# Optimization experiments

Hardware: AMD Instinct MI355X
Metric: run time of the kernel (lower is better)

The kernel has to match this reference:

```python
import jax, jax.numpy as jnp
import numpy as np

BETA = 0.25  # VQ commitment cost


def setup_inputs() -> dict:
    key = jax.random.key(0)
    ks = jax.random.split(key, 6)
    B, C, H, W = 4096, 10, 32, 32
    Din, D, K = 3 * H * W, 256, 512
    img = jax.random.normal(ks[0], (B, 3, H, W), jnp.float32)
    label = jax.random.randint(ks[1], (B,), 0, C)
    enc_W = jax.random.normal(ks[2], (C, Din, D), jnp.float32) * (1.0 / np.sqrt(Din))
    enc_b = jnp.zeros((C, D), jnp.float32)
    codebook = jax.random.normal(ks[3], (K, D), jnp.float32)
    dec_W = jax.random.normal(ks[4], (D, Din), jnp.float32) * (1.0 / np.sqrt(D))
    dec_b = jnp.zeros((Din,), jnp.float32)
    return {"img": img, "label": label, "enc_W": enc_W, "enc_b": enc_b,
            "codebook": codebook, "dec_W": dec_W, "dec_b": dec_b}


def reference(img, label, enc_W, enc_b, codebook, dec_W, dec_b):
    B = img.shape[0]
    C = enc_W.shape[0]
    x = img.reshape(B, -1)                                   # [B, Din]
    onehot = jax.nn.one_hot(label, C, dtype=x.dtype)         # [B, C]
    # label-routed per-class encoders: encode with every expert, select by label
    z_all = jnp.einsum('bi,cid->bcd', x, enc_W) + enc_b[None]  # [B, C, D]
    z = jnp.einsum('bcd,bc->bd', z_all, onehot)              # [B, D]
    # --- VQ quantizer (shared) ---
    d2 = (jnp.sum(z * z, -1, keepdims=True)
          - 2.0 * (z @ codebook.T)
          + jnp.sum(codebook * codebook, -1)[None])          # [B, K]
    idx = jnp.argmin(d2, axis=-1)                            # [B]
    q = codebook[idx]                                        # [B, D]
    # per-sample VQ loss (mean over latent dim): codebook + beta*commitment
    cb_l = jnp.mean((jax.lax.stop_gradient(z) - q) ** 2, -1)
    cm_l = jnp.mean((z - jax.lax.stop_gradient(q)) ** 2, -1)
    l = cb_l + BETA * cm_l                                   # [B]
    q_st = z + jax.lax.stop_gradient(q - z)                  # straight-through
    # quantization loss = (sum over activated classes of per-subset mean) / n_activated
    counts = jax.ops.segment_sum(jnp.ones((B,), x.dtype), label, num_segments=C)
    sum_l = jax.ops.segment_sum(l, label, num_segments=C)
    present = counts > 0
    per_class = jnp.where(present, sum_l / jnp.maximum(counts, 1.0), 0.0)
    n_act = jnp.maximum(jnp.sum(present.astype(x.dtype)), 1.0)
    quant = jnp.sum(per_class) / n_act
    # shared decoder; scatter-back is identity here since every label has an expert
    dec = q_st @ dec_W + dec_b                               # [B, Din]
    img_out = dec.reshape(img.shape)
    loss = jnp.mean((img_out - img) ** 2) + quant
    return (loss, img_out)
```

## Files before the change

kernel.cpp:

```cpp
#include <hip/hip_runtime.h>
#include <hip/hip_bf16.h>
#include <stddef.h>
#include <stdint.h>

#define NB   4096
#define NC   10
#define DIN  3072
#define DD   256
#define KCB  512
#define KSPLIT 6
#define KC   (DIN / KSPLIT)
#define TM   128
#define TGRID 42
#define NIT  (KC / 32)

#define PW_C  786432
#define PW_NH 393216
#define PW_KS 65536
#define PW_IT 4096

typedef unsigned short u16;
typedef short s16x8 __attribute__((ext_vector_type(8)));
typedef float f32x4 __attribute__((ext_vector_type(4)));

__device__ inline void f2bf2(float f, u16& h, u16& l) {
    unsigned uf = __builtin_bit_cast(unsigned, f);
    unsigned uh = (uf + 0x7FFFu + ((uf >> 16) & 1u)) >> 16;
    h = (u16)uh;
    float fh = __builtin_bit_cast(float, uh << 16);
    float r = f - fh;
    unsigned ur = __builtin_bit_cast(unsigned, r);
    l = (u16)((ur + 0x7FFFu + ((ur >> 16) & 1u)) >> 16);
}

__device__ __forceinline__ void gl16(const u16* g, u16* l) {
    __builtin_amdgcn_global_load_lds(
        (const __attribute__((address_space(1))) unsigned int*)(uintptr_t)g,
        (__attribute__((address_space(3))) unsigned int*)(unsigned int)(uintptr_t)l,
        16, 0, 0);
}

__global__ __launch_bounds__(256) void k_wtp(
    const int* __restrict__ label, const float* __restrict__ cb,
    const float* __restrict__ encW, const float* __restrict__ dW,
    int* __restrict__ meta, int* __restrict__ order, float* __restrict__ cbn,
    u16* __restrict__ WtH, u16* __restrict__ WtL,
    u16* __restrict__ dWtH, u16* __restrict__ dWtL, float* __restrict__ cbt)
{
    const int t = threadIdx.x;
    const int bid = blockIdx.x;
    if (bid == 0) {
        __shared__ int cnt_s[NC], cur_s[NC], off_s[NC];
        if (t < NC) { cnt_s[t] = 0; cur_s[t] = 0; }
        __syncthreads();
        for (int b = t; b < NB; b += 256) atomicAdd(&cnt_s[label[b]], 1);
        __syncthreads();
        if (t == 0) {
            int o = 0;
            for (int c = 0; c < NC; ++c) {
                off_s[c] = o; meta[c] = cnt_s[c]; meta[32 + c] = o; o += cnt_s[c];
            }
            meta[32 + NC] = o;
            int ntl = 0;
            for (int c = 0; c < NC; ++c)
                for (int r0 = 0; r0 < cnt_s[c]; r0 += TM) {
                    meta[64 + 2 * ntl] = c; meta[65 + 2 * ntl] = r0; ++ntl;
                }
            meta[63] = ntl;
        }
        __syncthreads();
        for (int b = t; b < NB; b += 256) {
            int c = label[b];
            int p = atomicAdd(&cur_s[c], 1);
            order[off_s[c] + p] = b;
        }
        return;
    }
    if (bid <= 2) {
        int k = (bid - 1) * 256 + t;
        if (k < KCB) {
            const float* r = cb + (size_t)k * DD;
            float a = 0.f;
#pragma unroll 4
            for (int i = 0; i < 64; ++i) {
                float4 v = *(const float4*)(r + i * 4);
                a = fmaf(v.x, v.x, fmaf(v.y, v.y, fmaf(v.z, v.z, fmaf(v.w, v.w, a))));
            }
            cbn[k] = a;
        }
        return;
    }
    const int wb = bid - 3;
    const float* src; int lsrc, ldst, k0, n0;
    u16 *dH = nullptr, *dL = nullptr; float* fdst = nullptr;
    int encw_c = -1;
    if (wb < 1920) {
        int c = wb / 192, rem = wb % 192;
        int kt = rem >> 2, nt = rem & 3;
        k0 = kt * 64; n0 = nt * 64;
        src = encW + (size_t)c * DIN * DD;  lsrc = DD;
        encw_c = c; ldst = 0;
    } else if (wb < 2112) {
        int rem = wb - 1920;
        int kt = rem / 48, nt = rem % 48;
        k0 = kt * 64; n0 = nt * 64;
        src = dW; lsrc = DIN;
        dH = dWtH; dL = dWtL; ldst = DD;
    } else {
        int rem = wb - 2112;
        int kt = rem >> 2, nt = rem & 3;
        k0 = kt * 64; n0 = nt * 64;
        src = cb; lsrc = DD;
        fdst = cbt; ldst = KCB;
    }
    __shared__ float tile[64][65];
    const int trow = t >> 4, tc4 = t & 15;
#pragma unroll
    for (int j = 0; j < 4; ++j) {
        int kk = trow * 4 + j;
        float4 v = *(const float4*)&src[(size_t)(k0 + kk) * lsrc + n0 + tc4 * 4];
        tile[kk][tc4 * 4 + 0] = v.x; tile[kk][tc4 * 4 + 1] = v.y;
        tile[kk][tc4 * 4 + 2] = v.z; tile[kk][tc4 * 4 + 3] = v.w;
    }
    __syncthreads();
    const int n = n0 + (t >> 2), q = t & 3;
    if (fdst) {
#pragma unroll
        for (int j = 0; j < 4; ++j) {
            float4 o = {tile[q * 16 + 4 * j + 0][n - n0], tile[q * 16 + 4 * j + 1][n - n0],
                        tile[q * 16 + 4 * j + 2][n - n0], tile[q * 16 + 4 * j + 3][n - n0]};
            *(float4*)&fdst[(size_t)n * ldst + k0 + q * 16 + 4 * j] = o;
        }
        return;
    }
    s16x8 vh0, vh1, vl0, vl1;
#pragma unroll
    for (int i = 0; i < 8; ++i) {
        u16 h, l;
        f2bf2(tile[q * 16 + i][n - n0], h, l);
        vh0[i] = (short)h; vl0[i] = (short)l;
    }
#pragma unroll
    for (int i = 0; i < 8; ++i) {
        u16 h, l;
        f2bf2(tile[q * 16 + 8 + i][n - n0], h, l);
        vh1[i] = (short)h; vl1[i] = (short)l;
    }
    if (encw_c >= 0) {
        const int nh = n >> 7, cg = (n & 127) >> 4, fr2 = n & 15;
        const size_t nbase = (size_t)encw_c * PW_C + (size_t)nh * PW_NH
                           + (size_t)cg * 512 + (size_t)fr2 * 8;
        int ko = (k0 >> 3) + 2 * q;
        {
            int ks2 = ko >> 6, r2 = ko & 63, it2 = r2 >> 2, fg2 = r2 & 3;
            size_t o = nbase + (size_t)ks2 * PW_KS + (size_t)it2 * PW_IT + (size_t)fg2 * 128;
            *(s16x8*)&WtH[o] = vh0; *(s16x8*)&WtL[o] = vl0;
        }
        {
            int ko1 = ko + 1;
            int ks2 = ko1 >> 6, r2 = ko1 & 63, it2 = r2 >> 2, fg2 = r2 & 3;
            size_t o = nbase + (size_t)ks2 * PW_KS + (size_t)it2 * PW_IT + (size_t)fg2 * 128;
            *(s16x8*)&WtH[o] = vh1; *(s16x8*)&WtL[o] = vl1;
        }
        return;
    }
    u16* oH = dH + (size_t)n * ldst + k0 + q * 16;
    u16* oL = dL + (size_t)n * ldst + k0 + q * 16;
    *(s16x8*)oH = vh0; *(s16x8*)(oH + 8) = vh1;
    *(s16x8*)oL = vl0; *(s16x8*)(oL + 8) = vl1;
}

#define ENC_STEP(IT, PB, L0, L1, C0, C1)                                        \
    {                                                                           \
        if ((IT) + 1 < NIT) { asm volatile("s_waitcnt vmcnt(6)" ::: "memory"); } \
        else                { asm volatile("s_waitcnt vmcnt(0)" ::: "memory"); } \
        asm volatile("s_waitcnt lgkmcnt(0)" ::: "memory");                      \
        __builtin_amdgcn_s_barrier();                                           \
        __builtin_amdgcn_sched_barrier(0);                                      \
        s16x8 aH[4], aL[4], bH[4], bL[4];                                       \
        _Pragma("unroll")                                                       \
        for (int mt = 0; mt < 4; ++mt) {                                        \
            aH[mt] = *(const s16x8*)&AsH[(wr * 4 + mt) * 512 + arb];            \
            aL[mt] = *(const s16x8*)&AsL[(wr * 4 + mt) * 512 + arb];            \
        }                                                                       \
        _Pragma("unroll")                                                       \
        for (int ct = 0; ct < 4; ++ct) {                                        \
            bH[ct] = *(const s16x8*)&BsH[PB][ct * 512 + brb];                   \
            bL[ct] = *(const s16x8*)&BsL[PB][ct * 512 + brb];                   \
        }                                                                       \
        asm volatile("s_waitcnt lgkmcnt(0)" ::: "memory");                      \
        __builtin_amdgcn_sched_barrier(0);                                      \
        __builtin_amdgcn_s_barrier();                                           \
        __builtin_amdgcn_sched_barrier(0);                                      \
        if ((IT) + 2 < NIT) {                                                   \
            L0 = *(const float4*)(xp + ((IT) + 2) * 32);                        \
            L1 = *(const float4*)(xp + ((IT) + 2) * 32 + 4);                    \
            __builtin_amdgcn_sched_barrier(0);                                  \
            const u16* g_ = gchunk + (size_t)((IT) + 2) * PW_IT;                \
            u16* l_ = lchunk + (PB) * 8192;                                     \
            _Pragma("unroll")                                                   \
            for (int i = 0; i < 4; ++i) gl16(g_ + i * 512, l_ + i * 512);       \
            __builtin_amdgcn_sched_barrier(0);                                  \
        }                                                                       \
        __builtin_amdgcn_s_setprio(1);                                          \
        _Pragma("unroll")                                                       \
        for (int ct = 0; ct < 4; ++ct) {                                        \
            _Pragma("unroll")                                                   \
            for (int mt = 0; mt < 4; ++mt) {                                    \
                acc[mt][ct] = __builtin_amdgcn_mfma_f32_16x16x32_bf16(aH[mt], bH[ct], acc[mt][ct], 0, 0, 0); \
                acc[mt][ct] = __builtin_amdgcn_mfma_f32_16x16x32_bf16(aL[mt], bH[ct], acc[mt][ct], 0, 0, 0); \
                acc[mt][ct] = __builtin_amdgcn_mfma_f32_16x16x32_bf16(aH[mt], bL[ct], acc[mt][ct], 0, 0, 0); \
            }                                                                   \
        }                                                                       \
        __builtin_amdgcn_s_setprio(0);                                          \
        if ((IT) + 1 < NIT) {                                                   \
            if ((IT) + 2 < NIT) { asm volatile("s_waitcnt vmcnt(10)" ::: "memory"); } \
            else                { asm volatile("s_waitcnt vmcnt(4)"  ::: "memory"); } \
            cvt_store(C0, C1);                                                  \
        }                                                                       \
    }

__global__ __launch_bounds__(512, 2) void k_enc(
    const float* __restrict__ x, const u16* __restrict__ WpH, const u16* __restrict__ WpL,
    const int* __restrict__ order, const int* __restrict__ meta, float* __restrict__ zpart)
{
    const int bid = blockIdx.x;
    const int ks  = bid % KSPLIT;
    const int tid = bid / KSPLIT;
    if (tid >= meta[63]) return;
    const int c    = meta[64 + 2 * tid];
    const int row0 = meta[65 + 2 * tid];
    const int cnt  = meta[c];
    const int off  = meta[32 + c];
    const int kbase = ks * KC;

    __shared__ __align__(16) u16 AsH[4096], AsL[4096];
    __shared__ __align__(16) u16 BsH[2][8192], BsL[2][8192];

    const int t = threadIdx.x;
    const int lane = t & 63;
    const int w    = t >> 6;
    const int wr = w >> 2, wc = w & 3;
    const int fr = lane & 15, fg = lane >> 4;

    const int ar = ((t >> 6) << 4) | (t & 15);
    const int aq = (t >> 4) & 3;
    int lr = row0 + ar; if (lr > cnt - 1) lr = cnt - 1;
    const float* xp = x + (size_t)order[off + lr] * DIN + kbase + aq * 8;
    const int aoffs = t * 8;

    const u16* gchunk = ((w >> 2) ? WpL : WpH)
                      + (size_t)c * PW_C + (size_t)(w & 1) * PW_NH
                      + (size_t)ks * PW_KS + ((w >> 1) & 1) * 2048 + lane * 8;
    u16* lchunk = ((w >> 2) ? &BsL[0][0] : &BsH[0][0])
                + (w & 1) * 4096 + ((w >> 1) & 1) * 2048 + lane * 8;

    f32x4 acc[4][4];
#pragma unroll
    for (int i = 0; i < 4; ++i)
#pragma unroll
        for (int j = 0; j < 4; ++j) acc[i][j] = (f32x4){0.f, 0.f, 0.f, 0.f};

    auto cvt_store = [&](float4 a0, float4 a1) {
        float av[8] = {a0.x, a0.y, a0.z, a0.w, a1.x, a1.y, a1.z, a1.w};
        s16x8 vh, vl;
#pragma unroll
        for (int i = 0; i < 8; ++i) {
            u16 h, l; f2bf2(av[i], h, l);
            vh[i] = (short)h; vl[i] = (short)l;
        }
        *(s16x8*)&AsH[aoffs] = vh;
        *(s16x8*)&AsL[aoffs] = vl;
    };

    const int arb = fg * 128 + fr * 8;
    const int brb = (wc >> 1) * 4096 + (wc & 1) * 2048 + arb;

    float4 sa0, sa1, sb0, sb1;

    sa0 = *(const float4*)xp;
    sa1 = *(const float4*)(xp + 4);
    __builtin_amdgcn_sched_barrier(0);
#pragma unroll
    for (int i = 0; i < 4; ++i) gl16(gchunk + i * 512, lchunk + i * 512);
    __builtin_amdgcn_sched_barrier(0);
    asm volatile("s_waitcnt vmcnt(4)" ::: "memory");
    cvt_store(sa0, sa1);
    __builtin_amdgcn_sched_barrier(0);
    sb0 = *(const float4*)(xp + 32);
    sb1 = *(const float4*)(xp + 36);
    __builtin_amdgcn_sched_barrier(0);
#pragma unroll
    for (int i = 0; i < 4; ++i) gl16(gchunk + PW_IT + i * 512, lchunk + 8192 + i * 512);
    __builtin_amdgcn_sched_barrier(0);

    for (int itp = 0; itp < NIT; itp += 2) {
        ENC_STEP(itp,     0, sa0, sa1, sb0, sb1);
        ENC_STEP(itp + 1, 1, sb0, sb1, sa0, sa1);
    }

    float* zp = zpart + (size_t)ks * NB * DD;
#pragma unroll
    for (int mt = 0; mt < 4; ++mt) {
#pragma unroll
        for (int r = 0; r < 4; ++r) {
            int lrow = row0 + wr * 64 + mt * 16 + fg * 4 + r;
            if (lrow < cnt) {
                int gb = order[off + lrow];
                float* dst = zp + (size_t)gb * DD + wc * 64 + fr;
#pragma unroll
                for (int ct = 0; ct < 4; ++ct)
                    dst[ct * 16] = acc[mt][ct][r];
            }
        }
    }
}

__global__ __launch_bounds__(256, 3) void k_dec(
    const float* __restrict__ cb, const u16* __restrict__ dWtH, const u16* __restrict__ dWtL,
    const float* __restrict__ db, float* __restrict__ dcb)
{
    const int col0 = blockIdx.x * 256;
    const int m0   = blockIdx.y * 64;

    __shared__ u16 AsH[64 * 40], AsL[64 * 40], BsH[256 * 40], BsL[256 * 40];

    const int t = threadIdx.x;
    const int lane = t & 63;
    const int wid  = t >> 6;
    const int wr = wid >> 1, wc = wid & 1;

    const int ar = t >> 2, aq = t & 3;
    const float* ap = cb + (size_t)(m0 + ar) * DD + aq * 8;
    const int bc = t >> 1, bh = t & 1;
    const u16* wH0 = dWtH + (size_t)(col0 + bc) * DD + bh * 16;
    const u16* wH1 = wH0 + (size_t)128 * DD;
    const u16* wL0 = dWtL + (size_t)(col0 + bc) * DD + bh * 16;
    const u16* wL1 = wL0 + (size_t)128 * DD;

    f32x4 acc[2][8];
#pragma unroll
    for (int i = 0; i < 2; ++i)
#pragma unroll
        for (int j = 0; j < 8; ++j) acc[i][j] = (f32x4){0.f, 0.f, 0.f, 0.f};

    const int fr = lane & 15, fg = lane >> 4;
    const int aoff = fg * 8;
    const int awr = ar * 40 + aq * 8;
    const int bw0 = bc * 40 + bh * 16;
    const int bw1 = (bc + 128) * 40 + bh * 16;

    float4 pa0 = *(const float4*)(ap);
    float4 pa1 = *(const float4*)(ap + 4);
    s16x8 ph0 = *(const s16x8*)(wH0);
    s16x8 ph1 = *(const s16x8*)(wH0 + 8);
    s16x8 ph2 = *(const s16x8*)(wH1);
    s16x8 ph3 = *(const s16x8*)(wH1 + 8);
    s16x8 pl0 = *(const s16x8*)(wL0);
    s16x8 pl1 = *(const s16x8*)(wL0 + 8);
    s16x8 pl2 = *(const s16x8*)(wL1);
    s16x8 pl3 = *(const s16x8*)(wL1 + 8);

    for (int it = 0; it < DD / 32; ++it) {
        {
            float av[8] = {pa0.x, pa0.y, pa0.z, pa0.w, pa1.x, pa1.y, pa1.z, pa1.w};
            s16x8 vh, vl;
#pragma unroll
            for (int i = 0; i < 8; ++i) {
                u16 h, l; f2bf2(av[i], h, l);
                vh[i] = (short)h; vl[i] = (short)l;
            }
            *(s16x8*)&AsH[awr] = vh;
            *(s16x8*)&AsL[awr] = vl;
            *(s16x8*)&BsH[bw0]     = ph0;
            *(s16x8*)&BsH[bw0 + 8] = ph1;
            *(s16x8*)&BsH[bw1]     = ph2;
            *(s16x8*)&BsH[bw1 + 8] = ph3;
            *(s16x8*)&BsL[bw0]     = pl0;
            *(s16x8*)&BsL[bw0 + 8] = pl1;
            *(s16x8*)&BsL[bw1]     = pl2;
            *(s16x8*)&BsL[bw1 + 8] = pl3;
        }
        __syncthreads();
        if (it + 1 < DD / 32) {
            const int k0 = (it + 1) * 32;
            pa0 = *(const float4*)(ap + k0);
            pa1 = *(const float4*)(ap + k0 + 4);
            ph0 = *(const s16x8*)(wH0 + k0);
            ph1 = *(const s16x8*)(wH0 + k0 + 8);
            ph2 = *(const s16x8*)(wH1 + k0);
            ph3 = *(const s16x8*)(wH1 + k0 + 8);
            pl0 = *(const s16x8*)(wL0 + k0);
            pl1 = *(const s16x8*)(wL0 + k0 + 8);
            pl2 = *(const s16x8*)(wL1 + k0);
            pl3 = *(const s16x8*)(wL1 + k0 + 8);
        }
        s16x8 aH0 = *(const s16x8*)&AsH[(wr * 32 + fr) * 40 + aoff];
        s16x8 aH1 = *(const s16x8*)&AsH[(wr * 32 + 16 + fr) * 40 + aoff];
        s16x8 aL0 = *(const s16x8*)&AsL[(wr * 32 + fr) * 40 + aoff];
        s16x8 aL1 = *(const s16x8*)&AsL[(wr * 32 + 16 + fr) * 40 + aoff];
#pragma unroll
        for (int nt = 0; nt < 8; ++nt) {
            const int bcol = wc * 128 + nt * 16 + fr;
            s16x8 bH = *(const s16x8*)&BsH[bcol * 40 + aoff];
            s16x8 bL = *(const s16x8*)&BsL[bcol * 40 + aoff];
            acc[0][nt] = __builtin_amdgcn_mfma_f32_16x16x32_bf16(aH0, bH, acc[0][nt], 0, 0, 0);
            acc[0][nt] = __builtin_amdgcn_mfma_f32_16x16x32_bf16(aL0, bH, acc[0][nt], 0, 0, 0);
            acc[0][nt] = __builtin_amdgcn_mfma_f32_16x16x32_bf16(aH0, bL, acc[0][nt], 0, 0, 0);
            acc[1][nt] = __builtin_amdgcn_mfma_f32_16x16x32_bf16(aH1, bH, acc[1][nt], 0, 0, 0);
            acc[1][nt] = __builtin_amdgcn_mfma_f32_16x16x32_bf16(aL1, bH, acc[1][nt], 0, 0, 0);
            acc[1][nt] = __builtin_amdgcn_mfma_f32_16x16x32_bf16(aH1, bL, acc[1][nt], 0, 0, 0);
        }
        __syncthreads();
    }

#pragma unroll
    for (int mt = 0; mt < 2; ++mt) {
#pragma unroll
        for (int r = 0; r < 4; ++r) {
            int grow = m0 + wr * 32 + mt * 16 + fg * 4 + r;
            float* dst = dcb + (size_t)grow * DIN + col0 + wc * 128 + fr;
#pragma unroll
            for (int nt = 0; nt < 8; ++nt)
                dst[nt * 16] = acc[mt][nt][r] + db[col0 + wc * 128 + nt * 16 + fr];
        }
    }
}

__global__ __launch_bounds__(256) void k_zred(
    const float* __restrict__ zpart, const float* __restrict__ encB,
    const int* __restrict__ label, float* __restrict__ z, float* __restrict__ zn)
{
    int id = blockIdx.x * 256 + threadIdx.x;
    int b = id >> 6, c4 = id & 63;
    int lab = label[b];
    float4 s = *(const float4*)&encB[lab * DD + c4 * 4];
    const float* p = zpart + (size_t)b * DD + c4 * 4;
#pragma unroll
    for (int ks = 0; ks < KSPLIT; ++ks) {
        float4 v = *(const float4*)(p + (size_t)ks * NB * DD);
        s.x += v.x; s.y += v.y; s.z += v.z; s.w += v.w;
    }
    *(float4*)&z[(size_t)b * DD + c4 * 4] = s;
    float sq = fmaf(s.x, s.x, fmaf(s.y, s.y, fmaf(s.z, s.z, s.w * s.w)));
#pragma unroll
    for (int o = 32; o > 0; o >>= 1) sq += __shfl_down(sq, o, 64);
    if ((threadIdx.x & 63) == 0) zn[b] = sq;
}

__global__ __launch_bounds__(256) void k_vq(
    const float* __restrict__ z, const float* __restrict__ cbt, const float* __restrict__ cbn,
    float* __restrict__ vmin, int* __restrict__ vidx)
{
    const int sg = blockIdx.x >> 2;
    const int q  = blockIdx.x & 3;
    const int b0 = sg * 32;
    const int code0 = q * 128;

    __shared__ float As[32][36];
    __shared__ float Bs[32][132];

    const int t = threadIdx.x;
    const int tx = t & 31, ty = t >> 5;

    const int ar = t >> 3, akq = t & 7;
    const float* zp = z + (size_t)(b0 + ar) * DD + akq * 4;
    const int bkk = t >> 3, bcq = t & 7;
    const float* cp = cbt + (size_t)bkk * KCB + code0 + bcq * 16;

    float acc[4][4];
#pragma unroll
    for (int i = 0; i < 4; ++i)
#pragma unroll
        for (int j = 0; j < 4; ++j) acc[i][j] = 0.f;

    float4 pa  = *(const float4*)zp;
    float4 pb0 = *(const float4*)(cp);
    float4 pb1 = *(const float4*)(cp + 4);
    float4 pb2 = *(const float4*)(cp + 8);
    float4 pb3 = *(const float4*)(cp + 12);

    for (int it = 0; it < DD / 32; ++it) {
        As[akq * 4 + 0][ar] = pa.x;
        As[akq * 4 + 1][ar] = pa.y;
        As[akq * 4 + 2][ar] = pa.z;
        As[akq * 4 + 3][ar] = pa.w;
        *(float4*)&Bs[bkk][bcq * 16]      = pb0;
        *(float4*)&Bs[bkk][bcq * 16 + 4]  = pb1;
        *(float4*)&Bs[bkk][bcq * 16 + 8]  = pb2;
        *(float4*)&Bs[bkk][bcq * 16 + 12] = pb3;
        __syncthreads();
        if (it + 1 < DD / 32) {
            const float* zpn = zp + (it + 1) * 32;
            const float* cpn = cp + (size_t)(it + 1) * 32 * KCB;
            pa  = *(const float4*)zpn;
            pb0 = *(const float4*)(cpn);
            pb1 = *(const float4*)(cpn + 4);
            pb2 = *(const float4*)(cpn + 8);
            pb3 = *(const float4*)(cpn + 12);
        }
#pragma unroll
        for (int kk = 0; kk < 32; ++kk) {
            float4 a4 = *(const float4*)&As[kk][ty * 4];
            float4 b4 = *(const float4*)&Bs[kk][tx * 4];
            float am[4] = {a4.x, a4.y, a4.z, a4.w};
            float bn[4] = {b4.x, b4.y, b4.z, b4.w};
#pragma unroll
            for (int i = 0; i < 4; ++i)
#pragma unroll
                for (int j = 0; j < 4; ++j)
                    acc[i][j] = fmaf(am[i], bn[j], acc[i][j]);
        }
        __syncthreads();
    }

    float4 cn4 = *(const float4*)&cbn[code0 + tx * 4];
    float cnv[4] = {cn4.x, cn4.y, cn4.z, cn4.w};
#pragma unroll
    for (int i = 0; i < 4; ++i) {
        float m = cnv[0] - 2.f * acc[i][0];
        int bi = code0 + tx * 4;
#pragma unroll
        for (int j = 1; j < 4; ++j) {
            float sc = cnv[j] - 2.f * acc[i][j];
            if (sc < m) { m = sc; bi = code0 + tx * 4 + j; }
        }
#pragma unroll
        for (int mask = 1; mask <= 16; mask <<= 1) {
            float om = __shfl_xor(m, mask, 64);
            int   oi = __shfl_xor(bi, mask, 64);
            bool lowerSelf = (tx & mask) == 0;
            float lm = lowerSelf ? m : om;
            int   li = lowerSelf ? bi : oi;
            float hm = lowerSelf ? om : m;
            int   hi2 = lowerSelf ? oi : bi;
            if (hm < lm) { m = hm; bi = hi2; } else { m = lm; bi = li; }
        }
        if (tx == 0) {
            vmin[(size_t)(b0 + ty * 4 + i) * 4 + q] = m;
            vidx[(size_t)(b0 + ty * 4 + i) * 4 + q] = bi;
        }
    }
}

__global__ __launch_bounds__(256) void k_gather(
    const float* __restrict__ dcb, const float* __restrict__ vmin, const int* __restrict__ vidx,
    const float* __restrict__ zn, const float* __restrict__ img,
    float* __restrict__ out1, float* __restrict__ ssep, float* __restrict__ lo)
{
    const int b = blockIdx.x;
    float m = vmin[(size_t)b * 4]; int k = vidx[(size_t)b * 4];
#pragma unroll
    for (int q = 1; q < 4; ++q) {
        float v = vmin[(size_t)b * 4 + q];
        if (v < m) { m = v; k = vidx[(size_t)b * 4 + q]; }
    }
    if (threadIdx.x == 0) lo[b] = (zn[b] + m) * (1.25f / 256.f);

    const float* src = dcb + (size_t)k * DIN;
    const float* im  = img + (size_t)b * DIN;
    float* o = out1 + (size_t)b * DIN;
    const float4* s4 = (const float4*)src;
    const float4* i4 = (const float4*)im;

    float accv = 0.f;
#pragma unroll
    for (int j = 0; j < 3; ++j) {
        int i = threadIdx.x + j * 256;
        float4 v = s4[i], w = i4[i];
        float dx = v.x - w.x, dy = v.y - w.y, dz = v.z - w.z, dw = v.w - w.w;
        accv = fmaf(dx, dx, fmaf(dy, dy, fmaf(dz, dz, fmaf(dw, dw, accv))));
    }
#pragma unroll
    for (int j = 0; j < 3; ++j) {
        int i = threadIdx.x + j * 256;
        if (i < DIN / 4 - 1) {
            float4 a = s4[i], b2 = s4[i + 1];
            float4 ov = {a.w, b2.x, b2.y, b2.z};
            *(float4*)(o + 3 + 4 * i) = ov;
        }
    }
    if (threadIdx.x == 0) {
        o[0] = src[0]; o[1] = src[1]; o[2] = src[2];
        o[DIN - 1] = src[DIN - 1];
    }

    __shared__ float red[256];
    red[threadIdx.x] = accv;
    __syncthreads();
#pragma unroll
    for (int st = 128; st > 0; st >>= 1) {
        if (threadIdx.x < st) red[threadIdx.x] += red[threadIdx.x + st];
        __syncthreads();
    }
    if (threadIdx.x == 0) ssep[b] = red[0];
}

__global__ __launch_bounds__(256) void k_final(
    const float* __restrict__ ssep, const float* __restrict__ lo, const int* __restrict__ label,
    const int* __restrict__ meta, float* __restrict__ out)
{
    const int t = threadIdx.x;
    __shared__ float part[4][12];

    float se = 0.f;
    float la[NC];
#pragma unroll
    for (int c = 0; c < NC; ++c) la[c] = 0.f;
    for (int b = t; b < NB; b += 256) {
        se += ssep[b];
        int c2 = label[b]; float v = lo[b];
#pragma unroll
        for (int cc = 0; cc < NC; ++cc) la[cc] += (cc == c2) ? v : 0.f;
    }

#pragma unroll
    for (int o = 32; o > 0; o >>= 1) se += __shfl_down(se, o, 64);
#pragma unroll
    for (int cc = 0; cc < NC; ++cc) {
#pragma unroll
        for (int o = 32; o > 0; o >>= 1) la[cc] += __shfl_down(la[cc], o, 64);
    }
    if ((t & 63) == 0) {
        const int wv = t >> 6;
        part[wv][0] = se;
#pragma unroll
        for (int cc = 0; cc < NC; ++cc) part[wv][1 + cc] = la[cc];
    }
    __syncthreads();

    if (t == 0) {
        float sse = part[0][0] + part[1][0] + part[2][0] + part[3][0];
        float quant = 0.f, nact = 0.f;
        for (int cc = 0; cc < NC; ++cc) {
            float cs = part[0][1 + cc] + part[1][1 + cc] + part[2][1 + cc] + part[3][1 + cc];
            int cnt = meta[cc];
            if (cnt > 0) { quant += cs / (float)cnt; nact += 1.f; }
        }
        if (nact < 1.f) nact = 1.f;
        quant /= nact;
        out[0] = sse / (float)(NB * DIN) + quant;
    }
}

extern "C" void kernel_launch(void* const* d_in, const int* in_sizes, int n_in,
                              void* d_out, int out_size, void* d_ws, size_t ws_size,
                              hipStream_t stream)
{
    const float* img   = (const float*)d_in[0];
    const int*   label = (const int*)d_in[1];
    const float* encW  = (const float*)d_in[2];
    const float* encB  = (const float*)d_in[3];
    const float* cb    = (const float*)d_in[4];
    const float* dW    = (const float*)d_in[5];
    const float* db    = (const float*)d_in[6];
    float* out = (float*)d_out;

    char* w = (char*)d_ws;
    float* zpart = (float*)(w);
    float* dcb   = (float*)(w);
    float* z     = (float*)(w + 33554432);
    u16*   WtH   = (u16*)  (w + 37748736);
    u16*   WtL   = (u16*)  (w + 53477376);
    u16*   dWtH  = (u16*)  (w + 69206016);
    u16*   dWtL  = (u16*)  (w + 70778880);
    float* vmin  = (float*)(w + 72351744);
    int*   vidx  = (int*)  (w + 72417280);
    float* zn    = (float*)(w + 72482816);
    float* lo    = (float*)(w + 72499200);
    float* ssep  = (float*)(w + 72515584);
    int*   order = (int*)  (w + 72548352);
    int*   meta  = (int*)  (w + 72564736);
    float* cbn   = (float*)(w + 72568832);
    float* cbt   = (float*)(w + 72570880);

    hipLaunchKernelGGL(k_wtp,    dim3(2147),           dim3(256), 0, stream,
                       label, cb, encW, dW, meta, order, cbn, WtH, WtL, dWtH, dWtL, cbt);
    hipLaunchKernelGGL(k_enc,    dim3(TGRID * KSPLIT), dim3(512), 0, stream, img, WtH, WtL, order, meta, zpart);
    hipLaunchKernelGGL(k_zred,   dim3(1024),           dim3(256), 0, stream, zpart, encB, label, z, zn);
    hipLaunchKernelGGL(k_vq,     dim3(512),            dim3(256), 0, stream, z, cbt, cbn, vmin, vidx);
    hipLaunchKernelGGL(k_dec,    dim3(12, 8),          dim3(256), 0, stream, cb, dWtH, dWtL, db, dcb);
    hipLaunchKernelGGL(k_gather, dim3(4096),           dim3(256), 0, stream,
                       dcb, vmin, vidx, zn, img, out + 1, ssep, lo);
    hipLaunchKernelGGL(k_final,  dim3(1),              dim3(256), 0, stream, ssep, lo, label, meta, out);
}
```

Measured before the change: 127.6 us.

## Merge encoder and codebook-decoder GEMMs into one launch with heterogeneous blocks

```diff
diff --git a/kernel.cpp b/kernel.cpp
--- a/kernel.cpp
+++ b/kernel.cpp
@@ -13,6 +13,8 @@
 #define TM   128
 #define TGRID 42
 #define NIT  (KC / 32)
+#define NENC (TGRID * KSPLIT)
+#define NDEC 96
 
 #define PW_C  786432
 #define PW_NH 393216
@@ -21,6 +23,7 @@
 
 typedef unsigned short u16;
 typedef short s16x8 __attribute__((ext_vector_type(8)));
+typedef short s16x4 __attribute__((ext_vector_type(4)));
 typedef float f32x4 __attribute__((ext_vector_type(4)));
 
 __device__ inline void f2bf2(float f, u16& h, u16& l) {
@@ -220,209 +223,202 @@
         }                                                                       \
     }
 
-__global__ __launch_bounds__(512, 2) void k_enc(
+__global__ __launch_bounds__(512, 2) void k_encdec(
     const float* __restrict__ x, const u16* __restrict__ WpH, const u16* __restrict__ WpL,
-    const int* __restrict__ order, const int* __restrict__ meta, float* __restrict__ zpart)
-{
-    const int bid = blockIdx.x;
-    const int ks  = bid % KSPLIT;
-    const int tid = bid / KSPLIT;
-    if (tid >= meta[63]) return;
-    const int c    = meta[64 + 2 * tid];
-    const int row0 = meta[65 + 2 * tid];
-    const int cnt  = meta[c];
-    const int off  = meta[32 + c];
-    const int kbase = ks * KC;
-
-    __shared__ __align__(16) u16 AsH[4096], AsL[4096];
-    __shared__ __align__(16) u16 BsH[2][8192], BsL[2][8192];
-
-    const int t = threadIdx.x;
-    const int lane = t & 63;
-    const int w    = t >> 6;
-    const int wr = w >> 2, wc = w & 3;
-    const int fr = lane & 15, fg = lane >> 4;
-
-    const int ar = ((t >> 6) << 4) | (t & 15);
-    const int aq = (t >> 4) & 3;
-    int lr = row0 + ar; if (lr > cnt - 1) lr = cnt - 1;
-    const float* xp = x + (size_t)order[off + lr] * DIN + kbase + aq * 8;
-    const int aoffs = t * 8;
-
-    const u16* gchunk = ((w >> 2) ? WpL : WpH)
-                      + (size_t)c * PW_C + (size_t)(w & 1) * PW_NH
-                      + (size_t)ks * PW_KS + ((w >> 1) & 1) * 2048 + lane * 8;
-    u16* lchunk = ((w >> 2) ? &BsL[0][0] : &BsH[0][0])
-                + (w & 1) * 4096 + ((w >> 1) & 1) * 2048 + lane * 8;
-
-    f32x4 acc[4][4];
-#pragma unroll
-    for (int i = 0; i < 4; ++i)
-#pragma unroll
-        for (int j = 0; j < 4; ++j) acc[i][j] = (f32x4){0.f, 0.f, 0.f, 0.f};
-
-    auto cvt_store = [&](float4 a0, float4 a1) {
-        float av[8] = {a0.x, a0.y, a0.z, a0.w, a1.x, a1.y, a1.z, a1.w};
-        s16x8 vh, vl;
-#pragma unroll
-        for (int i = 0; i < 8; ++i) {
-            u16 h, l; f2bf2(av[i], h, l);
-            vh[i] = (short)h; vl[i] = (short)l;
-        }
-        *(s16x8*)&AsH[aoffs] = vh;
-        *(s16x8*)&AsL[aoffs] = vl;
-    };
-
-    const int arb = fg * 128 + fr * 8;
-    const int brb = (wc >> 1) * 4096 + (wc & 1) * 2048 + arb;
-
-    float4 sa0, sa1, sb0, sb1;
-
-    sa0 = *(const float4*)xp;
-    sa1 = *(const float4*)(xp + 4);
-    __builtin_amdgcn_sched_barrier(0);
-#pragma unroll
-    for (int i = 0; i < 4; ++i) gl16(gchunk + i * 512, lchunk + i * 512);
-    __builtin_amdgcn_sched_barrier(0);
-    asm volatile("s_waitcnt vmcnt(4)" ::: "memory");
-    cvt_store(sa0, sa1);
-    __builtin_amdgcn_sched_barrier(0);
-    sb0 = *(const float4*)(xp + 32);
-    sb1 = *(const float4*)(xp + 36);
-    __builtin_amdgcn_sched_barrier(0);
-#pragma unroll
-    for (int i = 0; i < 4; ++i) gl16(gchunk + PW_IT + i * 512, lchunk + 8192 + i * 512);
-    __builtin_amdgcn_sched_barrier(0);
-
-    for (int itp = 0; itp < NIT; itp += 2) {
-        ENC_STEP(itp,     0, sa0, sa1, sb0, sb1);
-        ENC_STEP(itp + 1, 1, sb0, sb1, sa0, sa1);
-    }
-
-    float* zp = zpart + (size_t)ks * NB * DD;
-#pragma unroll
-    for (int mt = 0; mt < 4; ++mt) {
-#pragma unroll
-        for (int r = 0; r < 4; ++r) {
-            int lrow = row0 + wr * 64 + mt * 16 + fg * 4 + r;
-            if (lrow < cnt) {
-                int gb = order[off + lrow];
-                float* dst = zp + (size_t)gb * DD + wc * 64 + fr;
-#pragma unroll
-                for (int ct = 0; ct < 4; ++ct)
-                    dst[ct * 16] = acc[mt][ct][r];
-            }
-        }
-    }
-}
-
-__global__ __launch_bounds__(256, 3) void k_dec(
+    const int* __restrict__ order, const int* __restrict__ meta, float* __restrict__ zpart,
     const float* __restrict__ cb, const u16* __restrict__ dWtH, const u16* __restrict__ dWtL,
     const float* __restrict__ db, float* __restrict__ dcb)
 {
-    const int col0 = blockIdx.x * 256;
-    const int m0   = blockIdx.y * 64;
-
-    __shared__ u16 AsH[64 * 40], AsL[64 * 40], BsH[256 * 40], BsL[256 * 40];
-
-    const int t = threadIdx.x;
-    const int lane = t & 63;
-    const int wid  = t >> 6;
-    const int wr = wid >> 1, wc = wid & 1;
-
-    const int ar = t >> 2, aq = t & 3;
-    const float* ap = cb + (size_t)(m0 + ar) * DD + aq * 8;
-    const int bc = t >> 1, bh = t & 1;
-    const u16* wH0 = dWtH + (size_t)(col0 + bc) * DD + bh * 16;
-    const u16* wH1 = wH0 + (size_t)128 * DD;
-    const u16* wL0 = dWtL + (size_t)(col0 + bc) * DD + bh * 16;
-    const u16* wL1 = wL0 + (size_t)128 * DD;
-
-    f32x4 acc[2][8];
-#pragma unroll
-    for (int i = 0; i < 2; ++i)
-#pragma unroll
-        for (int j = 0; j < 8; ++j) acc[i][j] = (f32x4){0.f, 0.f, 0.f, 0.f};
-
-    const int fr = lane & 15, fg = lane >> 4;
-    const int aoff = fg * 8;
-    const int awr = ar * 40 + aq * 8;
-    const int bw0 = bc * 40 + bh * 16;
-    const int bw1 = (bc + 128) * 40 + bh * 16;
-
-    float4 pa0 = *(const float4*)(ap);
-    float4 pa1 = *(const float4*)(ap + 4);
-    s16x8 ph0 = *(const s16x8*)(wH0);
-    s16x8 ph1 = *(const s16x8*)(wH0 + 8);
-    s16x8 ph2 = *(const s16x8*)(wH1);
-    s16x8 ph3 = *(const s16x8*)(wH1 + 8);
-    s16x8 pl0 = *(const s16x8*)(wL0);
-    s16x8 pl1 = *(const s16x8*)(wL0 + 8);
-    s16x8 pl2 = *(const s16x8*)(wL1);
-    s16x8 pl3 = *(const s16x8*)(wL1 + 8);
-
-    for (int it = 0; it < DD / 32; ++it) {
-        {
-            float av[8] = {pa0.x, pa0.y, pa0.z, pa0.w, pa1.x, pa1.y, pa1.z, pa1.w};
+    __shared__ __align__(16) u16 smem[40960];
+    const int bid = blockIdx.x;
+
+    if (bid < NENC) {
+        const int ks  = bid % KSPLIT;
+        const int tid = bid / KSPLIT;
+        if (tid >= meta[63]) return;
+        const int c    = meta[64 + 2 * tid];
+        const int row0 = meta[65 + 2 * tid];
+        const int cnt  = meta[c];
+        const int off  = meta[32 + c];
+        const int kbase = ks * KC;
+
+        u16* AsH = smem;
+        u16* AsL = smem + 4096;
+        u16 (*BsH)[8192] = (u16(*)[8192])(smem + 8192);
+        u16 (*BsL)[8192] = (u16(*)[8192])(smem + 24576);
+
+        const int t = threadIdx.x;
+        const int lane = t & 63;
+        const int w    = t >> 6;
+        const int wr = w >> 2, wc = w & 3;
+        const int fr = lane & 15, fg = lane >> 4;
+
+        const int ar = ((t >> 6) << 4) | (t & 15);
+        const int aq = (t >> 4) & 3;
+        int lr = row0 + ar; if (lr > cnt - 1) lr = cnt - 1;
+        const float* xp = x + (size_t)order[off + lr] * DIN + kbase + aq * 8;
+        const int aoffs = t * 8;
+
+        const u16* gchunk = ((w >> 2) ? WpL : WpH)
+                          + (size_t)c * PW_C + (size_t)(w & 1) * PW_NH
+                          + (size_t)ks * PW_KS + ((w >> 1) & 1) * 2048 + lane * 8;
+        u16* lchunk = ((w >> 2) ? &BsL[0][0] : &BsH[0][0])
+                    + (w & 1) * 4096 + ((w >> 1) & 1) * 2048 + lane * 8;
+
+        f32x4 acc[4][4];
+#pragma unroll
+        for (int i = 0; i < 4; ++i)
+#pragma unroll
+            for (int j = 0; j < 4; ++j) acc[i][j] = (f32x4){0.f, 0.f, 0.f, 0.f};
+
+        auto cvt_store = [&](float4 a0, float4 a1) {
+            float av[8] = {a0.x, a0.y, a0.z, a0.w, a1.x, a1.y, a1.z, a1.w};
             s16x8 vh, vl;
 #pragma unroll
             for (int i = 0; i < 8; ++i) {
                 u16 h, l; f2bf2(av[i], h, l);
                 vh[i] = (short)h; vl[i] = (short)l;
             }
-            *(s16x8*)&AsH[awr] = vh;
-            *(s16x8*)&AsL[awr] = vl;
-            *(s16x8*)&BsH[bw0]     = ph0;
-            *(s16x8*)&BsH[bw0 + 8] = ph1;
-            *(s16x8*)&BsH[bw1]     = ph2;
-            *(s16x8*)&BsH[bw1 + 8] = ph3;
-            *(s16x8*)&BsL[bw0]     = pl0;
-            *(s16x8*)&BsL[bw0 + 8] = pl1;
-            *(s16x8*)&BsL[bw1]     = pl2;
-            *(s16x8*)&BsL[bw1 + 8] = pl3;
-        }
-        __syncthreads();
-        if (it + 1 < DD / 32) {
-            const int k0 = (it + 1) * 32;
-            pa0 = *(const float4*)(ap + k0);
-            pa1 = *(const float4*)(ap + k0 + 4);
-            ph0 = *(const s16x8*)(wH0 + k0);
-            ph1 = *(const s16x8*)(wH0 + k0 + 8);
-            ph2 = *(const s16x8*)(wH1 + k0);
-            ph3 = *(const s16x8*)(wH1 + k0 + 8);
-            pl0 = *(const s16x8*)(wL0 + k0);
-            pl1 = *(const s16x8*)(wL0 + k0 + 8);
-            pl2 = *(const s16x8*)(wL1 + k0);
-            pl3 = *(const s16x8*)(wL1 + k0 + 8);
-        }
-        s16x8 aH0 = *(const s16x8*)&AsH[(wr * 32 + fr) * 40 + aoff];
-        s16x8 aH1 = *(const s16x8*)&AsH[(wr * 32 + 16 + fr) * 40 + aoff];
-        s16x8 aL0 = *(const s16x8*)&AsL[(wr * 32 + fr) * 40 + aoff];
-        s16x8 aL1 = *(const s16x8*)&AsL[(wr * 32 + 16 + fr) * 40 + aoff];
-#pragma unroll
-        for (int nt = 0; nt < 8; ++nt) {
-            const int bcol = wc * 128 + nt * 16 + fr;
-            s16x8 bH = *(const s16x8*)&BsH[bcol * 40 + aoff];
-            s16x8 bL = *(const s16x8*)&BsL[bcol * 40 + aoff];
-            acc[0][nt] = __builtin_amdgcn_mfma_f32_16x16x32_bf16(aH0, bH, acc[0][nt], 0, 0, 0);
-            acc[0][nt] = __builtin_amdgcn_mfma_f32_16x16x32_bf16(aL0, bH, acc[0][nt], 0, 0, 0);
-            acc[0][nt] = __builtin_amdgcn_mfma_f32_16x16x32_bf16(aH0, bL, acc[0][nt], 0, 0, 0);
-            acc[1][nt] = __builtin_amdgcn_mfma_f32_16x16x32_bf16(aH1, bH, acc[1][nt], 0, 0, 0);
-            acc[1][nt] = __builtin_amdgcn_mfma_f32_16x16x32_bf16(aL1, bH, acc[1][nt], 0, 0, 0);
-            acc[1][nt] = __builtin_amdgcn_mfma_f32_16x16x32_bf16(aH1, bL, acc[1][nt], 0, 0, 0);
-        }
-        __syncthreads();
-    }
-
-#pragma unroll
-    for (int mt = 0; mt < 2; ++mt) {
-#pragma unroll
-        for (int r = 0; r < 4; ++r) {
-            int grow = m0 + wr * 32 + mt * 16 + fg * 4 + r;
-            float* dst = dcb + (size_t)grow * DIN + col0 + wc * 128 + fr;
-#pragma unroll
-            for (int nt = 0; nt < 8; ++nt)
-                dst[nt * 16] = acc[mt][nt][r] + db[col0 + wc * 128 + nt * 16 + fr];
+            *(s16x8*)&AsH[aoffs] = vh;
+            *(s16x8*)&AsL[aoffs] = vl;
+        };
+
+        const int arb = fg * 128 + fr * 8;
+        const int brb = (wc >> 1) * 4096 + (wc & 1) * 2048 + arb;
+
+        float4 sa0, sa1, sb0, sb1;
+
+        sa0 = *(const float4*)xp;
+        sa1 = *(const float4*)(xp + 4);
+        __builtin_amdgcn_sched_barrier(0);
+#pragma unroll
+        for (int i = 0; i < 4; ++i) gl16(gchunk + i * 512, lchunk + i * 512);
+        __builtin_amdgcn_sched_barrier(0);
+        asm volatile("s_waitcnt vmcnt(4)" ::: "memory");
+        cvt_store(sa0, sa1);
+        __builtin_amdgcn_sched_barrier(0);
+        sb0 = *(const float4*)(xp + 32);
+        sb1 = *(const float4*)(xp + 36);
+        __builtin_amdgcn_sched_barrier(0);
+#pragma unroll
+        for (int i = 0; i < 4; ++i) gl16(gchunk + PW_IT + i * 512, lchunk + 8192 + i * 512);
+        __builtin_amdgcn_sched_barrier(0);
+
+        for (int itp = 0; itp < NIT; itp += 2) {
+            ENC_STEP(itp,     0, sa0, sa1, sb0, sb1);
+            ENC_STEP(itp + 1, 1, sb0, sb1, sa0, sa1);
+        }
+
+        float* zp = zpart + (size_t)ks * NB * DD;
+#pragma unroll
+        for (int mt = 0; mt < 4; ++mt) {
+#pragma unroll
+            for (int r = 0; r < 4; ++r) {
+                int lrow = row0 + wr * 64 + mt * 16 + fg * 4 + r;
+                if (lrow < cnt) {
+                    int gb = order[off + lrow];
+                    float* dst = zp + (size_t)gb * DD + wc * 64 + fr;
+#pragma unroll
+                    for (int ct = 0; ct < 4; ++ct)
+                        dst[ct * 16] = acc[mt][ct][r];
+                }
+            }
+        }
+        return;
+    }
+
+    {
+        const int bid2 = bid - NENC;
+        const int col0 = (bid2 % 12) * 256;
+        const int m0   = (bid2 / 12) * 64;
+
+        u16* AsH = smem;
+        u16* AsL = smem + 2560;
+        u16* BsH = smem + 5120;
+        u16* BsL = smem + 15360;
+
+        const int t = threadIdx.x;
+        const int lane = t & 63;
+        const int w8  = t >> 6;
+        const int wr = w8 >> 2, wc = w8 & 3;
+
+        const int ar = t >> 3, aq = t & 7;
+        const float* ap = cb + (size_t)(m0 + ar) * DD + aq * 4;
+        const int bc = t >> 1, bh = t & 1;
+        const u16* wH0 = dWtH + (size_t)(col0 + bc) * DD + bh * 16;
+        const u16* wL0 = dWtL + (size_t)(col0 + bc) * DD + bh * 16;
+
+        f32x4 acc[2][4];
+#pragma unroll
+        for (int i = 0; i < 2; ++i)
+#pragma unroll
+            for (int j = 0; j < 4; ++j) acc[i][j] = (f32x4){0.f, 0.f, 0.f, 0.f};
+
+        const int fr = lane & 15, fg = lane >> 4;
+        const int aoff = fg * 8;
+        const int awr = ar * 40 + aq * 4;
+        const int bw0 = bc * 40 + bh * 16;
+
+        float4 pa0 = *(const float4*)(ap);
+        s16x8 ph0 = *(const s16x8*)(wH0);
+        s16x8 ph1 = *(const s16x8*)(wH0 + 8);
+        s16x8 pl0 = *(const s16x8*)(wL0);
+        s16x8 pl1 = *(const s16x8*)(wL0 + 8);
+
+        for (int it = 0; it < DD / 32; ++it) {
+            {
+                float av[4] = {pa0.x, pa0.y, pa0.z, pa0.w};
+                s16x4 vh, vl;
+#pragma unroll
+                for (int i = 0; i < 4; ++i) {
+                    u16 h, l; f2bf2(av[i], h, l);
+                    vh[i] = (short)h; vl[i] = (short)l;
+                }
+                *(s16x4*)&AsH[awr] = vh;
+                *(s16x4*)&AsL[awr] = vl;
+                *(s16x8*)&BsH[bw0]     = ph0;
+                *(s16x8*)&BsH[bw0 + 8] = ph1;
+                *(s16x8*)&BsL[bw0]     = pl0;
+                *(s16x8*)&BsL[bw0 + 8] = pl1;
+            }
+            __syncthreads();
+            if (it + 1 < DD / 32) {
+                const int k0 = (it + 1) * 32;
+                pa0 = *(const float4*)(ap + k0);
+                ph0 = *(const s16x8*)(wH0 + k0);
+                ph1 = *(const s16x8*)(wH0 + k0 + 8);
+                pl0 = *(const s16x8*)(wL0 + k0);
+                pl1 = *(const s16x8*)(wL0 + k0 + 8);
+            }
+            s16x8 aH0 = *(const s16x8*)&AsH[(wr * 32 + fr) * 40 + aoff];
+            s16x8 aH1 = *(const s16x8*)&AsH[(wr * 32 + 16 + fr) * 40 + aoff];
+            s16x8 aL0 = *(const s16x8*)&AsL[(wr * 32 + fr) * 40 + aoff];
+            s16x8 aL1 = *(const s16x8*)&AsL[(wr * 32 + 16 + fr) * 40 + aoff];
+#pragma unroll
+            for (int nt = 0; nt < 4; ++nt) {
+                const int bcol = wc * 64 + nt * 16 + fr;
+                s16x8 bH = *(const s16x8*)&BsH[bcol * 40 + aoff];
+                s16x8 bL = *(const s16x8*)&BsL[bcol * 40 + aoff];
+                acc[0][nt] = __builtin_amdgcn_mfma_f32_16x16x32_bf16(aH0, bH, acc[0][nt], 0, 0, 0);
+                acc[0][nt] = __builtin_amdgcn_mfma_f32_16x16x32_bf16(aL0, bH, acc[0][nt], 0, 0, 0);
+                acc[0][nt] = __builtin_amdgcn_mfma_f32_16x16x32_bf16(aH0, bL, acc[0][nt], 0, 0, 0);
+                acc[1][nt] = __builtin_amdgcn_mfma_f32_16x16x32_bf16(aH1, bH, acc[1][nt], 0, 0, 0);
+                acc[1][nt] = __builtin_amdgcn_mfma_f32_16x16x32_bf16(aL1, bH, acc[1][nt], 0, 0, 0);
+                acc[1][nt] = __builtin_amdgcn_mfma_f32_16x16x32_bf16(aH1, bL, acc[1][nt], 0, 0, 0);
+            }
+            __syncthreads();
+        }
+
+#pragma unroll
+        for (int mt = 0; mt < 2; ++mt) {
+#pragma unroll
+            for (int r = 0; r < 4; ++r) {
+                int grow = m0 + wr * 32 + mt * 16 + fg * 4 + r;
+                float* dst = dcb + (size_t)grow * DIN + col0 + wc * 64 + fr;
+#pragma unroll
+                for (int nt = 0; nt < 4; ++nt)
+                    dst[nt * 16] = acc[mt][nt][r] + db[col0 + wc * 64 + nt * 16 + fr];
+            }
         }
     }
 }
@@ -658,7 +654,7 @@
 
     char* w = (char*)d_ws;
     float* zpart = (float*)(w);
-    float* dcb   = (float*)(w);
+    float* dcb   = (float*)(w + 25165824);
     float* z     = (float*)(w + 33554432);
     u16*   WtH   = (u16*)  (w + 37748736);
     u16*   WtL   = (u16*)  (w + 53477376);
@@ -674,13 +670,13 @@
     float* cbn   = (float*)(w + 72568832);
     float* cbt   = (float*)(w + 72570880);
 
-    hipLaunchKernelGGL(k_wtp,    dim3(2147),           dim3(256), 0, stream,
+    hipLaunchKernelGGL(k_wtp,    dim3(2147),        dim3(256), 0, stream,
                        label, cb, encW, dW, meta, order, cbn, WtH, WtL, dWtH, dWtL, cbt);
-    hipLaunchKernelGGL(k_enc,    dim3(TGRID * KSPLIT), dim3(512), 0, stream, img, WtH, WtL, order, meta, zpart);
-    hipLaunchKernelGGL(k_zred,   dim3(1024),           dim3(256), 0, stream, zpart, encB, label, z, zn);
-    hipLaunchKernelGGL(k_vq,     dim3(512),            dim3(256), 0, stream, z, cbt, cbn, vmin, vidx);
-    hipLaunchKernelGGL(k_dec,    dim3(12, 8),          dim3(256), 0, stream, cb, dWtH, dWtL, db, dcb);
-    hipLaunchKernelGGL(k_gather, dim3(4096),           dim3(256), 0, stream,
+    hipLaunchKernelGGL(k_encdec, dim3(NENC + NDEC), dim3(512), 0, stream,
+                       img, WtH, WtL, order, meta, zpart, cb, dWtH, dWtL, db, dcb);
+    hipLaunchKernelGGL(k_zred,   dim3(1024),        dim3(256), 0, stream, zpart, encB, label, z, zn);
+    hipLaunchKernelGGL(k_vq,     dim3(512),         dim3(256), 0, stream, z, cbt, cbn, vmin, vidx);
+    hipLaunchKernelGGL(k_gather, dim3(4096),        dim3(256), 0, stream,
                        dcb, vmin, vidx, zn, img, out + 1, ssep, lo);
-    hipLaunchKernelGGL(k_final,  dim3(1),              dim3(256), 0, stream, ssep, lo, label, meta, out);
-}
+    hipLaunchKernelGGL(k_final,  dim3(1),           dim3(256), 0, stream, ssep, lo, label, meta, out);
+}
```

Result: faster. 123.3 us (-3.3%).
